# Performance work log

Hardware: AMD Instinct MI355X
Metric: run time of the kernel (lower is better)

## Reference

```python
import jax, jax.numpy as jnp
import numpy as np


def setup_inputs() -> dict:
    key = jax.random.key(0)
    k1, k2, k3, k4 = jax.random.split(key, 4)
    N, K, P2 = 4096, 256, 96  # examples, freqs, 2*p
    z = jax.random.normal(k1, (N, K, P2), dtype=jnp.float32)
    sigma_1 = jax.random.normal(k2, (K, P2, P2), dtype=jnp.float32)
    sigma_2 = jax.random.normal(k3, (K, P2, P2), dtype=jnp.float32)
    weights = jax.random.normal(k4, (K, P2, P2), dtype=jnp.float32)
    return {"z": z, "sigma_1": sigma_1, "sigma_2": sigma_2,
            "weights": weights, "n_1": 500, "n_2": 400}


def reference(z, sigma_1, sigma_2, weights, n_1, n_2):
    # z: (N, K, 2p), weights/sigma_1: (K, 2p, 2p)
    P2 = z.shape[-1]
    const = jnp.log(jnp.float32(n_1) / jnp.float32(n_2))
    # quadratic form z^T W_j z, batched over (example, freq)
    quad = jnp.einsum('nfp,fpq,nfq->nf', z, weights, z)  # (N, K)
    # det(W_j @ Sigma1_j + I) per frequency (independent of example)
    A = jnp.matmul(weights, sigma_1) + jnp.eye(P2, dtype=z.dtype)  # (K, 2p, 2p)
    det = jnp.clip(jnp.linalg.det(A), 1e-5, 1e5)  # (K,)
    sum_freq = quad - jnp.log(det)[None, :]  # (N, K)
    out = sum_freq.sum(axis=-1) + const  # (N,)
    return out.reshape(-1, 1)
```

## Files before the change

### kernel.cpp

```cpp
#include <hip/hip_runtime.h>


typedef __attribute__((ext_vector_type(8))) short bf16x8;
typedef __attribute__((ext_vector_type(4))) float f32x4;

#define WFENCE() asm volatile("" ::: "memory")

__device__ __forceinline__ unsigned short f2bf(float x) {
  unsigned int u = __builtin_bit_cast(unsigned int, x);
  u += 0x7fffu + ((u >> 16) & 1u);
  return (unsigned short)(u >> 16);
}
__device__ __forceinline__ float bf2f(unsigned short h) {
  unsigned int u = ((unsigned int)h) << 16;
  return __builtin_bit_cast(float, u);
}

#define ALD 100
#define WLD 35
#define ZLD 104

__device__ __forceinline__ void det_body(const int tid, const int f,
                                         const float* __restrict__ W,
                                         const float* __restrict__ S1,
                                         float* __restrict__ logdet,
                                         float* smem) {
  float* Wc = smem;
  float* Sc = smem + 3360;
  float* Al = smem;

  const int lane = tid & 63;
  const float* Wg = W + (size_t)f * 9216;
  const float* Sg = S1 + (size_t)f * 9216;

  const int i0 = (tid >> 3) * 3;
  const int j0 = (tid & 7) * 12;

  float acc[3][12];
#pragma unroll
  for (int a = 0; a < 3; ++a)
#pragma unroll
    for (int b = 0; b < 12; ++b) acc[a][b] = 0.f;

  for (int kc = 0; kc < 3; ++kc) {
#pragma unroll
    for (int it = 0; it < 3; ++it) {
      int c = tid + it * 256;
      int i = c >> 3;
      int k4 = (c & 7) << 2;
      const float4 v =
          *reinterpret_cast<const float4*>(Wg + i * 96 + kc * 32 + k4);
      Wc[i * WLD + k4 + 0] = v.x;
      Wc[i * WLD + k4 + 1] = v.y;
      Wc[i * WLD + k4 + 2] = v.z;
      Wc[i * WLD + k4 + 3] = v.w;
    }
#pragma unroll
    for (int it = 0; it < 3; ++it) {
      int c = tid + it * 256;
      int kk = c / 24;
      int j4 = (c % 24) << 2;
      const float4 v =
          *reinterpret_cast<const float4*>(Sg + (kc * 32 + kk) * 96 + j4);
      *reinterpret_cast<float4*>(&Sc[kk * 100 + j4]) = v;
    }
    __syncthreads();
#pragma unroll 2
    for (int kk = 0; kk < 32; ++kk) {
      float wv[3];
#pragma unroll
      for (int r = 0; r < 3; ++r) wv[r] = Wc[(i0 + r) * WLD + kk];
      float sv[12];
      const float4 s0 = *reinterpret_cast<const float4*>(&Sc[kk * 100 + j0]);
      const float4 s1 =
          *reinterpret_cast<const float4*>(&Sc[kk * 100 + j0 + 4]);
      const float4 s2 =
          *reinterpret_cast<const float4*>(&Sc[kk * 100 + j0 + 8]);
      sv[0] = s0.x; sv[1] = s0.y; sv[2] = s0.z; sv[3] = s0.w;
      sv[4] = s1.x; sv[5] = s1.y; sv[6] = s1.z; sv[7] = s1.w;
      sv[8] = s2.x; sv[9] = s2.y; sv[10] = s2.z; sv[11] = s2.w;
#pragma unroll
      for (int a = 0; a < 3; ++a)
#pragma unroll
        for (int b = 0; b < 12; ++b) acc[a][b] += wv[a] * sv[b];
    }
    __syncthreads();
  }

#pragma unroll
  for (int a = 0; a < 3; ++a) {
    int i = i0 + a;
#pragma unroll
    for (int c4 = 0; c4 < 3; ++c4) {
      float4 v;
      v.x = acc[a][c4 * 4 + 0] + ((i == j0 + c4 * 4 + 0) ? 1.f : 0.f);
      v.y = acc[a][c4 * 4 + 1] + ((i == j0 + c4 * 4 + 1) ? 1.f : 0.f);
      v.z = acc[a][c4 * 4 + 2] + ((i == j0 + c4 * 4 + 2) ? 1.f : 0.f);
      v.w = acc[a][c4 * 4 + 3] + ((i == j0 + c4 * 4 + 3) ? 1.f : 0.f);
      *reinterpret_cast<float4*>(&Al[i * ALD + j0 + c4 * 4]) = v;
    }
  }
  __syncthreads();

  float ls = 0.f;
  int neg = 0;
  int sgn = 0;

  for (int p = 0; p < 12; ++p) {
    const int c0 = p * 8;
    const int NC = 88 - c0;
    const int NT = NC >> 2;

    if (tid < 64) {
      const bool e0 = lane <= 95 - c0;
      const bool e1 = (c0 < 32) && (lane <= 31 - c0);
      float P0[8], P1[8];
#pragma unroll
      for (int m = 0; m < 8; ++m) { P0[m] = 0.f; P1[m] = 0.f; }
      if (e0) {
        const float4 x =
            *reinterpret_cast<const float4*>(&Al[(c0 + lane) * ALD + c0]);
        const float4 y =
            *reinterpret_cast<const float4*>(&Al[(c0 + lane) * ALD + c0 + 4]);
        P0[0] = x.x; P0[1] = x.y; P0[2] = x.z; P0[3] = x.w;
        P0[4] = y.x; P0[5] = y.y; P0[6] = y.z; P0[7] = y.w;
      }
      if (e1) {
        const float4 x = *reinterpret_cast<const float4*>(
            &Al[(c0 + 64 + lane) * ALD + c0]);
        const float4 y = *reinterpret_cast<const float4*>(
            &Al[(c0 + 64 + lane) * ALD + c0 + 4]);
        P1[0] = x.x; P1[1] = x.y; P1[2] = x.z; P1[3] = x.w;
        P1[4] = y.x; P1[5] = y.y; P1[6] = y.z; P1[7] = y.w;
      }

#pragma unroll
      for (int j = 0; j < 8; ++j) {
        const int jc = c0 + j;
        float pv;
        int tried = 0;
        for (;;) {
          pv = __shfl(P0[j], j);
          if (fabsf(pv) >= 1e-3f || tried) break;
          tried = 1;
          unsigned k0 = (e0 && lane >= j)
                            ? ((__float_as_uint(fabsf(P0[j])) & ~127u) |
                               (unsigned)lane)
                            : 0u;
          unsigned k1 = e1 ? ((__float_as_uint(fabsf(P1[j])) & ~127u) | 64u |
                              (unsigned)lane)
                           : 0u;
          unsigned key = k0 > k1 ? k0 : k1;
#pragma unroll
          for (int m = 1; m < 64; m <<= 1) {
            unsigned o = (unsigned)__shfl_xor((int)key, m);
            key = key > o ? key : o;
          }
          const int wl = (int)(key & 63u);
          const int slot = (int)((key >> 6) & 1u);
          const int bi = c0 + slot * 64 + wl;
          if (bi <= jc) break;
          sgn ^= 1;
#pragma unroll
          for (int m = 0; m < 8; ++m) {
            const float vj = __shfl(P0[m], j);
            const float vb0 = __shfl(P0[m], wl);
            const float vb1 = __shfl(P1[m], wl);
            const float vb = slot ? vb1 : vb0;
            if (lane == j) P0[m] = vb;
            if (lane == wl) {
              if (slot) P1[m] = vj;
              else P0[m] = vj;
            }
          }
          if (lane < NT) {
            const int col0 = c0 + 8 + lane * 4;
            float4 xx = *reinterpret_cast<float4*>(&Al[jc * ALD + col0]);
            float4 yy = *reinterpret_cast<float4*>(&Al[bi * ALD + col0]);
            *reinterpret_cast<float4*>(&Al[jc * ALD + col0]) = yy;
            *reinterpret_cast<float4*>(&Al[bi * ALD + col0]) = xx;
          }
          WFENCE();
        }
        const float rpv = __builtin_amdgcn_rcpf(pv);
        const bool up0 = e0 && (lane > j);
        const float L0 = P0[j] * rpv;
        const float L1 = P1[j] * rpv;
        if (up0) P0[j] = L0;
        if (e1) P1[j] = L1;
#pragma unroll
        for (int jj = j + 1; jj < 8; ++jj) {
          const float u = __shfl(P0[jj], j);
          if (up0) P0[jj] -= L0 * u;
          if (e1) P1[jj] -= L1 * u;
        }
        ls += logf(fabsf(pv));
        if (pv < 0.f) neg ^= 1;
      }
      if (e0) {
        float4 x = {P0[0], P0[1], P0[2], P0[3]};
        float4 y = {P0[4], P0[5], P0[6], P0[7]};
        *reinterpret_cast<float4*>(&Al[(c0 + lane) * ALD + c0]) = x;
        *reinterpret_cast<float4*>(&Al[(c0 + lane) * ALD + c0 + 4]) = y;
      }
      if (e1) {
        float4 x = {P1[0], P1[1], P1[2], P1[3]};
        float4 y = {P1[4], P1[5], P1[6], P1[7]};
        *reinterpret_cast<float4*>(&Al[(c0 + 64 + lane) * ALD + c0]) = x;
        *reinterpret_cast<float4*>(&Al[(c0 + 64 + lane) * ALD + c0 + 4]) = y;
      }
    }
    __syncthreads();

    if (NC > 0) {
      if (tid < NC) {
        const int ca = c0 + 8 + tid;
        float a[8];
#pragma unroll
        for (int i = 0; i < 8; ++i) a[i] = Al[(c0 + i) * ALD + ca];
#pragma unroll
        for (int jj = 1; jj < 8; ++jj)
#pragma unroll
          for (int i = 0; i < jj; ++i) {
            const float Lv = Al[(c0 + jj) * ALD + c0 + i];
            a[jj] -= Lv * a[i];
          }
#pragma unroll
        for (int i = 0; i < 8; ++i) Al[(c0 + i) * ALD + ca] = a[i];
      }
      __syncthreads();

      if (tid < NC) {
        const int r = c0 + 8 + tid;
        const float4 lx =
            *reinterpret_cast<const float4*>(&Al[r * ALD + c0]);
        const float4 ly =
            *reinterpret_cast<const float4*>(&Al[r * ALD + c0 + 4]);
        float Lr[8];
        Lr[0] = lx.x; Lr[1] = lx.y; Lr[2] = lx.z; Lr[3] = lx.w;
        Lr[4] = ly.x; Lr[5] = ly.y; Lr[6] = ly.z; Lr[7] = ly.w;
        for (int ct = 0; ct < NT; ++ct) {
          const int col0 = c0 + 8 + ct * 4;
          float4 u[8];
#pragma unroll
          for (int i = 0; i < 8; ++i)
            u[i] =
                *reinterpret_cast<const float4*>(&Al[(c0 + i) * ALD + col0]);
          float4 x = *reinterpret_cast<float4*>(&Al[r * ALD + col0]);
#pragma unroll
          for (int i = 0; i < 8; ++i) {
            x.x -= Lr[i] * u[i].x;
            x.y -= Lr[i] * u[i].y;
            x.z -= Lr[i] * u[i].z;
            x.w -= Lr[i] * u[i].w;
          }
          *reinterpret_cast<float4*>(&Al[r * ALD + col0]) = x;
        }
      }
    }
    __syncthreads();
  }

  if (tid == 0) {
    const float LMIN = -11.5129254f, LMAX = 11.5129254f;
    float c;
    if (neg ^ sgn) c = LMIN;
    else c = fminf(fmaxf(ls, LMIN), LMAX);
    logdet[f] = c;
  }
}

__device__ __forceinline__ void quad_body(const int tid, const int idx,
                                          const float* __restrict__ z,
                                          const float* __restrict__ W,
                                          float* __restrict__ partial,
                                          float* smem) {
  unsigned short* Zb = reinterpret_cast<unsigned short*>(smem);
  unsigned short* Wb = Zb + 128 * ZLD;

  const int lane = tid & 63, wave = tid >> 6;
  const int n0 = (idx & 31) * 128;
  const int f0 = (idx >> 5) * 16;
  const int lrow = lane & 15;
  const int lq = lane >> 4;
  const int lk8 = lq * 8;
  const int rgrp = tid >> 3;
  const int cgrp = tid & 7;

  float dotacc[2][4];
#pragma unroll
  for (int mt = 0; mt < 2; ++mt)
#pragma unroll
    for (int i = 0; i < 4; ++i) dotacc[mt][i] = 0.f;

  for (int ff = 0; ff < 16; ++ff) {
    const int f = f0 + ff;
#pragma unroll
    for (int p = 0; p < 4; ++p) {
      int r = p * 32 + rgrp;
      const float4* src = reinterpret_cast<const float4*>(
          z + (size_t)(n0 + r) * 24576 + (size_t)f * 96);
#pragma unroll
      for (int cc = 0; cc < 3; ++cc) {
        int c = cgrp + cc * 8;
        float4 d = src[c];
        ushort4 s;
        s.x = f2bf(d.x); s.y = f2bf(d.y); s.z = f2bf(d.z); s.w = f2bf(d.w);
        *reinterpret_cast<ushort4*>(&Zb[r * ZLD + c * 4]) = s;
      }
    }
    const float4* wsrc =
        reinterpret_cast<const float4*>(W + (size_t)f * 9216);
#pragma unroll
    for (int it = 0; it < 9; ++it) {
      int c = tid + it * 256;
      int k = c / 24, q4 = (c % 24) << 2;
      float4 d = wsrc[c];
      ushort4 s;
      s.x = f2bf(d.x); s.y = f2bf(d.y); s.z = f2bf(d.z); s.w = f2bf(d.w);
      *reinterpret_cast<ushort4*>(&Wb[k * ZLD + q4]) = s;
    }
    __syncthreads();

#pragma unroll
    for (int g = 0; g < 2; ++g) {
      f32x4 acc[2][3];
#pragma unroll
      for (int mt = 0; mt < 2; ++mt)
#pragma unroll
        for (int n3 = 0; n3 < 3; ++n3)
          acc[mt][n3] = (f32x4){0.f, 0.f, 0.f, 0.f};

#pragma unroll
      for (int ks = 0; ks < 3; ++ks) {
        bf16x8 a0 = *reinterpret_cast<const bf16x8*>(
            &Zb[(wave * 32 + lrow) * ZLD + ks * 32 + lk8]);
        bf16x8 a1 = *reinterpret_cast<const bf16x8*>(
            &Zb[(wave * 32 + 16 + lrow) * ZLD + ks * 32 + lk8]);
#pragma unroll
        for (int n3 = 0; n3 < 3; ++n3) {
          const int nt = g * 3 + n3;
          bf16x8 b = *reinterpret_cast<const bf16x8*>(
              &Wb[(nt * 16 + lrow) * ZLD + ks * 32 + lk8]);
          acc[0][n3] = __builtin_amdgcn_mfma_f32_16x16x32_bf16(a0, b,
                                                              acc[0][n3],
                                                              0, 0, 0);
          acc[1][n3] = __builtin_amdgcn_mfma_f32_16x16x32_bf16(a1, b,
                                                              acc[1][n3],
                                                              0, 0, 0);
        }
      }

#pragma unroll
      for (int mt = 0; mt < 2; ++mt) {
        int rbase = wave * 32 + mt * 16 + lq * 4;
#pragma unroll
        for (int i = 0; i < 4; ++i) {
          int row = rbase + i;
          float s = 0.f;
#pragma unroll
          for (int n3 = 0; n3 < 3; ++n3) {
            float zv = bf2f(Zb[row * ZLD + (g * 3 + n3) * 16 + lrow]);
            s += acc[mt][n3][i] * zv;
          }
          dotacc[mt][i] += s;
        }
      }
    }
    __syncthreads();
  }

#pragma unroll
  for (int mt = 0; mt < 2; ++mt)
#pragma unroll
    for (int i = 0; i < 4; ++i) {
      float v = dotacc[mt][i];
      v += __shfl_xor(v, 1);
      v += __shfl_xor(v, 2);
      v += __shfl_xor(v, 4);
      v += __shfl_xor(v, 8);
      dotacc[mt][i] = v;
    }
  if (lrow == 0) {
#pragma unroll
    for (int mt = 0; mt < 2; ++mt) {
      int row = wave * 32 + mt * 16 + lq * 4;
      float4 o = {dotacc[mt][0], dotacc[mt][1], dotacc[mt][2], dotacc[mt][3]};
      *reinterpret_cast<float4*>(
          &partial[(size_t)(idx >> 5) * 4096 + n0 + row]) = o;
    }
  }
}

__global__ __launch_bounds__(256, 4) void fused_kernel(
    const float* __restrict__ z, const float* __restrict__ W,
    const float* __restrict__ S1, float* __restrict__ partial,
    float* __restrict__ logdet) {
  __shared__ alignas(16) float smem[11648];
  if (blockIdx.x < 256) {
    det_body(threadIdx.x, blockIdx.x, W, S1, logdet, smem);
  } else {
    quad_body(threadIdx.x, blockIdx.x - 256, z, W, partial, smem);
  }
}

__global__ __launch_bounds__(256) void finalize_kernel(
    const float* __restrict__ partial, const float* __restrict__ logdet,
    const int* __restrict__ n1p, const int* __restrict__ n2p,
    float* __restrict__ out) {
  __shared__ float red[256];
  const int t = threadIdx.x;
  red[t] = logdet[t];
  __syncthreads();
  for (int s = 128; s > 0; s >>= 1) {
    if (t < s) red[t] += red[t + s];
    __syncthreads();
  }
  const float S = red[0];
  const int n = blockIdx.x * 256 + t;
  float acc = 0.f;
#pragma unroll
  for (int ft = 0; ft < 16; ++ft) acc += partial[ft * 4096 + n];
  const float cst = logf((float)(*n1p) / (float)(*n2p));
  out[n] = acc - S + cst;
}

extern "C" void kernel_launch(void* const* d_in, const int* in_sizes, int n_in,
                              void* d_out, int out_size, void* d_ws,
                              size_t ws_size, hipStream_t stream) {
  const float* z  = (const float*)d_in[0];
  const float* s1 = (const float*)d_in[1];
  const float* w  = (const float*)d_in[3];
  const int* n1   = (const int*)d_in[4];
  const int* n2   = (const int*)d_in[5];
  float* out      = (float*)d_out;

  char* ws = (char*)d_ws;
  float* partial = (float*)ws;
  float* logdet  = (float*)(ws + 262144);

  fused_kernel<<<dim3(768), dim3(256), 0, stream>>>(z, w, s1, partial, logdet);
  finalize_kernel<<<dim3(16), dim3(256), 0, stream>>>(partial, logdet, n1, n2,
                                                      out);
}
```

Measured before the change: 634.0 us.

## Prefetch next frequency's z tile into registers during MFMA compute

After: 556.1 us. 1.14x faster.

```diff
diff --git a/kernel.cpp b/kernel.cpp
--- a/kernel.cpp
+++ b/kernel.cpp
@@ -293,8 +293,8 @@
 #pragma unroll
     for (int i = 0; i < 4; ++i) dotacc[mt][i] = 0.f;
 
-  for (int ff = 0; ff < 16; ++ff) {
-    const int f = f0 + ff;
+  {
+    const int f = f0;
 #pragma unroll
     for (int p = 0; p < 4; ++p) {
       int r = p * 32 + rgrp;
@@ -321,15 +321,31 @@
       *reinterpret_cast<ushort4*>(&Wb[k * ZLD + q4]) = s;
     }
     __syncthreads();
-
-#pragma unroll
-    for (int g = 0; g < 2; ++g) {
-      f32x4 acc[2][3];
+  }
+
+  for (int ff = 0; ff < 16; ++ff) {
+    const int fn = f0 + ff + 1;
+
+    float4 zpre[12];
+    if (ff < 15) {
+#pragma unroll
+      for (int p = 0; p < 4; ++p) {
+        int r = p * 32 + rgrp;
+        const float4* src = reinterpret_cast<const float4*>(
+            z + (size_t)(n0 + r) * 24576 + (size_t)fn * 96);
+#pragma unroll
+        for (int cc = 0; cc < 3; ++cc) zpre[p * 3 + cc] = src[cgrp + cc * 8];
+      }
+    }
+
+#pragma unroll
+    for (int g = 0; g < 3; ++g) {
+      f32x4 acc[2][2];
 #pragma unroll
       for (int mt = 0; mt < 2; ++mt)
 #pragma unroll
-        for (int n3 = 0; n3 < 3; ++n3)
-          acc[mt][n3] = (f32x4){0.f, 0.f, 0.f, 0.f};
+        for (int n2 = 0; n2 < 2; ++n2)
+          acc[mt][n2] = (f32x4){0.f, 0.f, 0.f, 0.f};
 
 #pragma unroll
       for (int ks = 0; ks < 3; ++ks) {
@@ -338,15 +354,15 @@
         bf16x8 a1 = *reinterpret_cast<const bf16x8*>(
             &Zb[(wave * 32 + 16 + lrow) * ZLD + ks * 32 + lk8]);
 #pragma unroll
-        for (int n3 = 0; n3 < 3; ++n3) {
-          const int nt = g * 3 + n3;
+        for (int n2 = 0; n2 < 2; ++n2) {
+          const int nt = g * 2 + n2;
           bf16x8 b = *reinterpret_cast<const bf16x8*>(
               &Wb[(nt * 16 + lrow) * ZLD + ks * 32 + lk8]);
-          acc[0][n3] = __builtin_amdgcn_mfma_f32_16x16x32_bf16(a0, b,
-                                                              acc[0][n3],
+          acc[0][n2] = __builtin_amdgcn_mfma_f32_16x16x32_bf16(a0, b,
+                                                              acc[0][n2],
                                                               0, 0, 0);
-          acc[1][n3] = __builtin_amdgcn_mfma_f32_16x16x32_bf16(a1, b,
-                                                              acc[1][n3],
+          acc[1][n2] = __builtin_amdgcn_mfma_f32_16x16x32_bf16(a1, b,
+                                                              acc[1][n2],
                                                               0, 0, 0);
         }
       }
@@ -359,15 +375,46 @@
           int row = rbase + i;
           float s = 0.f;
 #pragma unroll
-          for (int n3 = 0; n3 < 3; ++n3) {
-            float zv = bf2f(Zb[row * ZLD + (g * 3 + n3) * 16 + lrow]);
-            s += acc[mt][n3][i] * zv;
+          for (int n2 = 0; n2 < 2; ++n2) {
+            float zv = bf2f(Zb[row * ZLD + (g * 2 + n2) * 16 + lrow]);
+            s += acc[mt][n2][i] * zv;
           }
           dotacc[mt][i] += s;
         }
       }
     }
     __syncthreads();
+
+    if (ff < 15) {
+      const float4* wsrc =
+          reinterpret_cast<const float4*>(W + (size_t)fn * 9216);
+      float4 wld[9];
+#pragma unroll
+      for (int it = 0; it < 9; ++it) wld[it] = wsrc[tid + it * 256];
+
+#pragma unroll
+      for (int p = 0; p < 4; ++p) {
+        int r = p * 32 + rgrp;
+#pragma unroll
+        for (int cc = 0; cc < 3; ++cc) {
+          int c = cgrp + cc * 8;
+          float4 d = zpre[p * 3 + cc];
+          ushort4 s;
+          s.x = f2bf(d.x); s.y = f2bf(d.y); s.z = f2bf(d.z); s.w = f2bf(d.w);
+          *reinterpret_cast<ushort4*>(&Zb[r * ZLD + c * 4]) = s;
+        }
+      }
+#pragma unroll
+      for (int it = 0; it < 9; ++it) {
+        int c = tid + it * 256;
+        int k = c / 24, q4 = (c % 24) << 2;
+        float4 d = wld[it];
+        ushort4 s;
+        s.x = f2bf(d.x); s.y = f2bf(d.y); s.z = f2bf(d.z); s.w = f2bf(d.w);
+        *reinterpret_cast<ushort4*>(&Wb[k * ZLD + q4]) = s;
+      }
+      __syncthreads();
+    }
   }
 
 #pragma unroll
```
